# Performance work log

Hardware: AMD Instinct MI355X
Metric: run time of the kernel (lower is better)

## Reference

```python
import jax, jax.numpy as jnp
import numpy as np

N = 50000        # nodes
E = 800000       # edges (avg degree 16)
IN = 256         # in_size
H = 4            # heads
C = 32           # out_size per head
NEG_SLOPE = 0.2  # PyG GATConv leaky_relu slope
LN_EPS = 1e-5


def setup_inputs() -> dict:
    key = jax.random.key(0)
    ks = jax.random.split(key, 6)
    x = jax.random.normal(ks[0], (N, IN), dtype=jnp.float32)
    edge_index = jax.random.randint(ks[1], (2, E), 0, N, dtype=jnp.int32)
    W = jax.random.normal(ks[2], (IN, H * C), dtype=jnp.float32) * 0.05
    att_src = jax.random.normal(ks[3], (H, C), dtype=jnp.float32) * 0.05
    att_dst = jax.random.normal(ks[4], (H, C), dtype=jnp.float32) * 0.05
    bias = jnp.zeros((H * C,), dtype=jnp.float32)
    ln_gamma = jnp.ones((H * C,), dtype=jnp.float32)
    ln_beta = jnp.zeros((H * C,), dtype=jnp.float32)
    return {"x": x, "edge_index": edge_index, "W": W, "att_src": att_src,
            "att_dst": att_dst, "bias": bias, "ln_gamma": ln_gamma,
            "ln_beta": ln_beta}


def _segment_softmax(alpha, seg, num_segments):
    # alpha: [E, H], softmax over edges sharing the same destination node.
    amax = jax.ops.segment_max(alpha, seg, num_segments=num_segments)  # [N, H]
    amax = jnp.where(jnp.isfinite(amax), amax, 0.0)  # nodes with no in-edges
    ex = jnp.exp(alpha - amax[seg])
    denom = jax.ops.segment_sum(ex, seg, num_segments=num_segments)    # [N, H]
    return ex / (denom[seg] + 1e-16)


def reference(x, edge_index, W, att_src, att_dst, bias, ln_gamma, ln_beta):
    # --- GATConv (concat=True) ---
    x_lin = (x @ W).reshape(N, H, C)                    # [N, H, C]
    a_src = jnp.sum(x_lin * att_src, axis=-1)           # [N, H]
    a_dst = jnp.sum(x_lin * att_dst, axis=-1)           # [N, H]
    src, dst = edge_index[0], edge_index[1]             # messages src -> dst
    alpha = a_src[src] + a_dst[dst]                     # [E, H]
    alpha = jnp.where(alpha >= 0, alpha, NEG_SLOPE * alpha)
    alpha = _segment_softmax(alpha, dst, N)             # [E, H]
    msg = x_lin[src] * alpha[..., None]                 # [E, H, C]
    out = jax.ops.segment_sum(msg, dst, num_segments=N) # [N, H, C]
    out = out.reshape(N, H * C) + bias                  # [N, H*C]
    # --- LayerNorm over feature dim ---
    mu = jnp.mean(out, axis=-1, keepdims=True)
    var = jnp.mean(jnp.square(out - mu), axis=-1, keepdims=True)
    out = (out - mu) * jax.lax.rsqrt(var + LN_EPS) * ln_gamma + ln_beta
    # --- activation ---
    return jax.nn.relu(out)
```

## Files before the change

kernel.cpp:

```cpp
#include <hip/hip_runtime.h>

#define NNODES 50000
#define NEDGES 800000
#define INFEAT 256
#define HC 128
#define NH 4
#define CPH 32
#define LSTRIDE 264

typedef unsigned int uint32;
typedef unsigned short u16;
typedef short short8 __attribute__((ext_vector_type(8)));
typedef float f32x4 __attribute__((ext_vector_type(4)));

__device__ __forceinline__ float b2f(u16 s) {
    uint32 u = ((uint32)s) << 16;
    return __builtin_bit_cast(float, u);
}
__device__ __forceinline__ u16 f2bf(float x) {
    uint32 u = __builtin_bit_cast(uint32, x);
    uint32 r = (u + 0x7FFFu + ((u >> 16) & 1u)) >> 16;
    return (u16)r;
}
__device__ __forceinline__ bool probe_bf16(const void* gamma) {
    return ((const uint32*)gamma)[0] == 0x3F803F80u;
}

__global__ __launch_bounds__(256) void wtp_kernel(const void* __restrict__ W,
                                                  const void* __restrict__ gm,
                                                  u16* __restrict__ wtp,
                                                  int* __restrict__ count) {
    const bool isbf = probe_bf16(gm);
    int c = blockIdx.x * 256 + threadIdx.x;
    int kt = c >> 9, nt = (c >> 6) & 7, l = c & 63;
    int r = l & 15, quad = l >> 4;
    int n = nt * 16 + r;
    int kbase = kt * 32 + quad * 8;
    u16 vals[8];
#pragma unroll
    for (int j = 0; j < 8; ++j) {
        int k = kbase + j;
        vals[j] = isbf ? ((const u16*)W)[k * HC + n] : f2bf(((const float*)W)[k * HC + n]);
    }
    *(uint4*)(wtp + (size_t)c * 8) = *(const uint4*)vals;
    for (int i = c; i < NNODES; i += 4096) count[i] = 0;
}

__global__ __launch_bounds__(256) void gemm_mfma(const void* __restrict__ x,
                                                 const uint4* __restrict__ wtp,
                                                 const void* __restrict__ att_src,
                                                 const void* __restrict__ att_dst,
                                                 const void* __restrict__ gm,
                                                 u16* __restrict__ xlin,
                                                 float* __restrict__ asrc,
                                                 float* __restrict__ adst) {
    __shared__ u16 atile[4 * 16 * LSTRIDE];
    const bool isbf = probe_bf16(gm);
    const int tid = threadIdx.x;
    const int wv = tid >> 6;
    const int lane = tid & 63;
    int wave = blockIdx.x * 4 + wv;
    int r = lane & 15;
    int quad = lane >> 4;
    int m0 = wave * 16;
    u16* my = atile + wv * (16 * LSTRIDE);

    if (isbf) {
#pragma unroll
        for (int rep = 0; rep < 8; ++rep) {
            int idx = rep * 64 + lane;
            int row = idx >> 5;
            int ch  = idx & 31;
            int gr = m0 + row;
            if (gr > NNODES - 1) gr = NNODES - 1;
            uint4 q = *(const uint4*)((const u16*)x + (size_t)gr * INFEAT + ch * 8);
            *(uint4*)(my + row * LSTRIDE + ch * 8) = q;
        }
    } else {
#pragma unroll
        for (int rep = 0; rep < 16; ++rep) {
            int idx = rep * 64 + lane;
            int row = idx >> 6;
            int c4  = idx & 63;
            int gr = m0 + row;
            if (gr > NNODES - 1) gr = NNODES - 1;
            float4 f = *(const float4*)((const float*)x + (size_t)gr * INFEAT + c4 * 4);
            u16 v[4] = {f2bf(f.x), f2bf(f.y), f2bf(f.z), f2bf(f.w)};
            *(uint2*)(my + row * LSTRIDE + c4 * 4) = *(const uint2*)v;
        }
    }
    __syncthreads();

    f32x4 acc[8];
#pragma unroll
    for (int nt = 0; nt < 8; ++nt) acc[nt] = (f32x4){0.f, 0.f, 0.f, 0.f};

#pragma unroll
    for (int kt = 0; kt < 8; ++kt) {
        short8 afrag = __builtin_bit_cast(short8,
            *(const uint4*)(my + r * LSTRIDE + kt * 32 + quad * 8));
#pragma unroll
        for (int nt = 0; nt < 8; ++nt) {
            short8 bfrag = __builtin_bit_cast(short8, wtp[(kt * 8 + nt) * 64 + lane]);
            acc[nt] = __builtin_amdgcn_mfma_f32_16x16x32_bf16(afrag, bfrag, acc[nt], 0, 0, 0);
        }
    }
#pragma unroll
    for (int nt = 0; nt < 8; ++nt) {
#pragma unroll
        for (int reg = 0; reg < 4; ++reg) {
            int grow = m0 + quad * 4 + reg;
            if (grow < NNODES) xlin[(size_t)grow * HC + nt * 16 + r] = f2bf(acc[nt][reg]);
        }
    }

    float asv[8], adv[8];
#pragma unroll
    for (int nt = 0; nt < 8; ++nt) {
        int c = nt * 16 + r;
        if (isbf) {
            asv[nt] = b2f(((const u16*)att_src)[c]);
            adv[nt] = b2f(((const u16*)att_dst)[c]);
        } else {
            asv[nt] = ((const float*)att_src)[c];
            adv[nt] = ((const float*)att_dst)[c];
        }
    }
    float psrc[4][4], pdst[4][4];
#pragma unroll
    for (int h = 0; h < 4; ++h)
#pragma unroll
        for (int reg = 0; reg < 4; ++reg) { psrc[h][reg] = 0.f; pdst[h][reg] = 0.f; }
#pragma unroll
    for (int nt = 0; nt < 8; ++nt) {
        const int h = nt >> 1;
#pragma unroll
        for (int reg = 0; reg < 4; ++reg) {
            psrc[h][reg] = fmaf(acc[nt][reg], asv[nt], psrc[h][reg]);
            pdst[h][reg] = fmaf(acc[nt][reg], adv[nt], pdst[h][reg]);
        }
    }
#pragma unroll
    for (int m = 1; m < 16; m <<= 1) {
#pragma unroll
        for (int h = 0; h < 4; ++h)
#pragma unroll
            for (int reg = 0; reg < 4; ++reg) {
                psrc[h][reg] += __shfl_xor(psrc[h][reg], m);
                pdst[h][reg] += __shfl_xor(pdst[h][reg], m);
            }
    }
#pragma unroll
    for (int reg = 0; reg < 4; ++reg)
#pragma unroll
        for (int h = 0; h < 4; ++h)
            if (r == reg * 4 + h) {
                int grow = m0 + quad * 4 + reg;
                if (grow < NNODES) {
                    asrc[grow * 4 + h] = psrc[h][reg];
                    adst[grow * 4 + h] = pdst[h][reg];
                }
            }
}

__global__ __launch_bounds__(256) void hist_kernel(const int* __restrict__ ei,
                                                   int* __restrict__ count,
                                                   int* __restrict__ rank) {
    int e = blockIdx.x * 256 + threadIdx.x;
    if (e < NEDGES) rank[e] = atomicAdd(&count[ei[NEDGES + e]], 1);
}

__global__ __launch_bounds__(256) void blkred_kernel(const int* __restrict__ count,
                                                     int* __restrict__ blksum) {
    int i = blockIdx.x * 256 + threadIdx.x;
    int v = (i < NNODES) ? count[i] : 0;
#pragma unroll
    for (int m = 1; m < 64; m <<= 1) v += __shfl_xor(v, m);
    __shared__ int s[4];
    if ((threadIdx.x & 63) == 0) s[threadIdx.x >> 6] = v;
    __syncthreads();
    if (threadIdx.x == 0) blksum[blockIdx.x] = s[0] + s[1] + s[2] + s[3];
}

__global__ __launch_bounds__(256) void scanout_kernel(const int* __restrict__ count,
                                                      const int* __restrict__ blksum,
                                                      int* __restrict__ offsets) {
    __shared__ int sb[256];
    __shared__ int sd[256];
    const int nblk = (NNODES + 255) / 256;
    int t = threadIdx.x;
    int bv = (t < nblk) ? blksum[t] : 0;
    sb[t] = bv;
    __syncthreads();
    for (int off = 1; off < 256; off <<= 1) {
        int tv = (t >= off) ? sb[t - off] : 0;
        __syncthreads();
        sb[t] += tv;
        __syncthreads();
    }
    int base = sb[blockIdx.x] - blksum[blockIdx.x];

    int i = blockIdx.x * 256 + t;
    int v = (i < NNODES) ? count[i] : 0;
    sd[t] = v;
    __syncthreads();
    for (int off = 1; off < 256; off <<= 1) {
        int tv = (t >= off) ? sd[t - off] : 0;
        __syncthreads();
        sd[t] += tv;
        __syncthreads();
    }
    if (i < NNODES) offsets[i] = base + sd[t] - v;
    if (i == 0) offsets[NNODES] = NEDGES;
}

__global__ __launch_bounds__(256) void scatter_kernel(const int* __restrict__ ei,
                                                      const int* __restrict__ offsets,
                                                      const int* __restrict__ rank,
                                                      int* __restrict__ col) {
    int e = blockIdx.x * 256 + threadIdx.x;
    if (e >= NEDGES) return;
    int d = ei[NEDGES + e];
    col[offsets[d] + rank[e]] = ei[e];
}

__global__ __launch_bounds__(256) void node_kernel(const u16* __restrict__ xlin,
                                                   const float* __restrict__ asrc,
                                                   const float* __restrict__ adst,
                                                   const int* __restrict__ offsets,
                                                   const int* __restrict__ col,
                                                   const void* __restrict__ bias,
                                                   const void* __restrict__ gamma,
                                                   const void* __restrict__ beta,
                                                   void* __restrict__ out) {
    const bool isbf = probe_bf16(gamma);
    int node = blockIdx.x * 4 + (threadIdx.x >> 6);
    int lane = threadIdx.x & 63;
    int h = lane >> 4;
    int f2 = lane * 2;
    float adh = adst[node * 4 + h];
    int start = offsets[node];
    int end = offsets[node + 1];

    float dsum = 0.f, acc0 = 0.f, acc1 = 0.f;
    for (int i = start; i < end; i += 8) {
        int cc[8];
        uint32 pf[8];
        float aw[8];
#pragma unroll
        for (int j = 0; j < 8; ++j) {
            int idx = i + j;
            cc[j] = col[idx < end ? idx : (end - 1)];
        }
#pragma unroll
        for (int j = 0; j < 8; ++j) {
            pf[j] = *(const uint32*)(xlin + (size_t)cc[j] * HC + f2);
            aw[j] = asrc[cc[j] * 4 + h];
        }
#pragma unroll
        for (int j = 0; j < 8; ++j) {
            float a = aw[j] + adh;
            a = (a >= 0.f) ? a : 0.2f * a;
            float w = (i + j < end) ? __expf(a) : 0.f;
            dsum += w;
            float x0 = __builtin_bit_cast(float, pf[j] << 16);
            float x1 = __builtin_bit_cast(float, pf[j] & 0xffff0000u);
            acc0 = fmaf(x0, w, acc0);
            acc1 = fmaf(x1, w, acc1);
        }
    }
    float rden = 1.f / (dsum + 1e-16f);

    float bi0, bi1, g0, g1, be0, be1;
    if (isbf) {
        uint32 bb = ((const uint32*)bias)[lane];
        uint32 gg = ((const uint32*)gamma)[lane];
        uint32 eb = ((const uint32*)beta)[lane];
        bi0 = b2f((u16)(bb & 0xffffu)); bi1 = b2f((u16)(bb >> 16));
        g0  = b2f((u16)(gg & 0xffffu)); g1  = b2f((u16)(gg >> 16));
        be0 = b2f((u16)(eb & 0xffffu)); be1 = b2f((u16)(eb >> 16));
    } else {
        float2 tb = ((const float2*)bias)[lane];
        float2 tg = ((const float2*)gamma)[lane];
        float2 te = ((const float2*)beta)[lane];
        bi0 = tb.x; bi1 = tb.y; g0 = tg.x; g1 = tg.y; be0 = te.x; be1 = te.y;
    }
    float v0 = fmaf(acc0, rden, bi0);
    float v1 = fmaf(acc1, rden, bi1);
    float s2 = v0 + v1;
    float q2 = v0 * v0 + v1 * v1;
#pragma unroll
    for (int m = 1; m < 64; m <<= 1) {
        s2 += __shfl_xor(s2, m);
        q2 += __shfl_xor(q2, m);
    }
    float mean = s2 * (1.f / 128.f);
    float var = q2 * (1.f / 128.f) - mean * mean;
    float inv = rsqrtf(var + 1e-5f);
    float d0 = v0 - mean, d1 = v1 - mean;
    float o0 = fmaxf(fmaf(d0 * inv, g0, be0), 0.f);
    float o1 = fmaxf(fmaf(d1 * inv, g1, be1), 0.f);
    if (isbf) {
        uint32 po = (uint32)f2bf(o0) | ((uint32)f2bf(o1) << 16);
        ((uint32*)out)[(size_t)node * 64 + lane] = po;
    } else {
        float2 po; po.x = o0; po.y = o1;
        ((float2*)out)[(size_t)node * 64 + lane] = po;
    }
}

extern "C" void kernel_launch(void* const* d_in, const int* in_sizes, int n_in,
                              void* d_out, int out_size, void* d_ws, size_t ws_size,
                              hipStream_t stream) {
    const void* x       = d_in[0];
    const int*  ei      = (const int*)d_in[1];
    const void* W       = d_in[2];
    const void* att_src = d_in[3];
    const void* att_dst = d_in[4];
    const void* bias    = d_in[5];
    const void* gamma   = d_in[6];
    const void* beta    = d_in[7];

    char* w = (char*)d_ws;
    size_t off = 0;
    u16* xlin    = (u16*)(w + off);   off += 12800000;
    u16* wtp     = (u16*)(w + off);   off += 65536;
    float* asrc  = (float*)(w + off); off += 800000;
    float* adst  = (float*)(w + off); off += 800000;
    int* count   = (int*)(w + off);   off += 200000;
    int* offsets = (int*)(w + off);   off += 200016;
    int* rank    = (int*)(w + off);   off += 3200000;
    int* blksum  = (int*)(w + off);   off += 1024;
    int* col     = (int*)(w + off);   off += 3200000;

    const int NBLK = (NNODES + 255) / 256;
    wtp_kernel<<<16, 256, 0, stream>>>(W, gamma, wtp, count);
    gemm_mfma<<<(NNODES + 63) / 64, 256, 0, stream>>>(x, (const uint4*)wtp, att_src, att_dst,
                                                      gamma, xlin, asrc, adst);
    hist_kernel<<<(NEDGES + 255) / 256, 256, 0, stream>>>(ei, count, rank);
    blkred_kernel<<<NBLK, 256, 0, stream>>>(count, blksum);
    scanout_kernel<<<NBLK, 256, 0, stream>>>(count, blksum, offsets);
    scatter_kernel<<<(NEDGES + 255) / 256, 256, 0, stream>>>(ei, offsets, rank, col);
    node_kernel<<<NNODES / 4, 256, 0, stream>>>(xlin, asrc, adst, offsets, col,
                                                bias, gamma, beta, d_out);
}
```

Before: 223.5 us.

## Fuse edge histogram into GEMM kernel and add exact-tail loops to aggregation

The separate histogram kernel is removed. Its atomic in-degree counting and rank assignment now run at the end of the GEMM kernel, with each block handling 1024 edges. This saves a launch and lets the atomics overlap with GEMM work, though it lengthens the GEMM kernel's tail. The node aggregation loop no longer pads to multiples of 8 with clamped redundant gathers. It now uses 8-wide, 4-wide and scalar remainder loops, which cuts wasted xlin/asrc loads and removes per-element bounds checks, at the cost of more code.

After: 215.6 us. -3.5%, faster.

```diff
diff --git a/kernel.cpp b/kernel.cpp
--- a/kernel.cpp
+++ b/kernel.cpp
@@ -53,7 +53,10 @@
                                                  const void* __restrict__ gm,
                                                  u16* __restrict__ xlin,
                                                  float* __restrict__ asrc,
-                                                 float* __restrict__ adst) {
+                                                 float* __restrict__ adst,
+                                                 const int* __restrict__ ei,
+                                                 int* __restrict__ count,
+                                                 int* __restrict__ rank) {
     __shared__ u16 atile[4 * 16 * LSTRIDE];
     const bool isbf = probe_bf16(gm);
     const int tid = threadIdx.x;
@@ -161,13 +164,13 @@
                     adst[grow * 4 + h] = pdst[h][reg];
                 }
             }
-}
-
-__global__ __launch_bounds__(256) void hist_kernel(const int* __restrict__ ei,
-                                                   int* __restrict__ count,
-                                                   int* __restrict__ rank) {
-    int e = blockIdx.x * 256 + threadIdx.x;
-    if (e < NEDGES) rank[e] = atomicAdd(&count[ei[NEDGES + e]], 1);
+
+    int eb = blockIdx.x * 1024 + tid;
+#pragma unroll
+    for (int rep = 0; rep < 4; ++rep) {
+        int e = eb + rep * 256;
+        if (e < NEDGES) rank[e] = atomicAdd(&count[ei[NEDGES + e]], 1);
+    }
 }
 
 __global__ __launch_bounds__(256) void blkred_kernel(const int* __restrict__ count,
@@ -243,15 +246,13 @@
     int end = offsets[node + 1];
 
     float dsum = 0.f, acc0 = 0.f, acc1 = 0.f;
-    for (int i = start; i < end; i += 8) {
+    int i = start;
+    for (; i + 7 < end; i += 8) {
         int cc[8];
         uint32 pf[8];
         float aw[8];
 #pragma unroll
-        for (int j = 0; j < 8; ++j) {
-            int idx = i + j;
-            cc[j] = col[idx < end ? idx : (end - 1)];
-        }
+        for (int j = 0; j < 8; ++j) cc[j] = col[i + j];
 #pragma unroll
         for (int j = 0; j < 8; ++j) {
             pf[j] = *(const uint32*)(xlin + (size_t)cc[j] * HC + f2);
@@ -261,13 +262,48 @@
         for (int j = 0; j < 8; ++j) {
             float a = aw[j] + adh;
             a = (a >= 0.f) ? a : 0.2f * a;
-            float w = (i + j < end) ? __expf(a) : 0.f;
+            float w = __expf(a);
             dsum += w;
             float x0 = __builtin_bit_cast(float, pf[j] << 16);
             float x1 = __builtin_bit_cast(float, pf[j] & 0xffff0000u);
             acc0 = fmaf(x0, w, acc0);
             acc1 = fmaf(x1, w, acc1);
         }
+    }
+    for (; i + 3 < end; i += 4) {
+        int cc[4];
+        uint32 pf[4];
+        float aw[4];
+#pragma unroll
+        for (int j = 0; j < 4; ++j) cc[j] = col[i + j];
+#pragma unroll
+        for (int j = 0; j < 4; ++j) {
+            pf[j] = *(const uint32*)(xlin + (size_t)cc[j] * HC + f2);
+            aw[j] = asrc[cc[j] * 4 + h];
+        }
+#pragma unroll
+        for (int j = 0; j < 4; ++j) {
+            float a = aw[j] + adh;
+            a = (a >= 0.f) ? a : 0.2f * a;
+            float w = __expf(a);
+            dsum += w;
+            float x0 = __builtin_bit_cast(float, pf[j] << 16);
+            float x1 = __builtin_bit_cast(float, pf[j] & 0xffff0000u);
+            acc0 = fmaf(x0, w, acc0);
+            acc1 = fmaf(x1, w, acc1);
+        }
+    }
+    for (; i < end; ++i) {
+        int c = col[i];
+        uint32 p = *(const uint32*)(xlin + (size_t)c * HC + f2);
+        float a = asrc[c * 4 + h] + adh;
+        a = (a >= 0.f) ? a : 0.2f * a;
+        float w = __expf(a);
+        dsum += w;
+        float x0 = __builtin_bit_cast(float, p << 16);
+        float x1 = __builtin_bit_cast(float, p & 0xffff0000u);
+        acc0 = fmaf(x0, w, acc0);
+        acc1 = fmaf(x1, w, acc1);
     }
     float rden = 1.f / (dsum + 1e-16f);
 
@@ -336,8 +372,8 @@
     const int NBLK = (NNODES + 255) / 256;
     wtp_kernel<<<16, 256, 0, stream>>>(W, gamma, wtp, count);
     gemm_mfma<<<(NNODES + 63) / 64, 256, 0, stream>>>(x, (const uint4*)wtp, att_src, att_dst,
-                                                      gamma, xlin, asrc, adst);
-    hist_kernel<<<(NEDGES + 255) / 256, 256, 0, stream>>>(ei, count, rank);
+                                                      gamma, xlin, asrc, adst,
+                                                      ei, count, rank);
     blkred_kernel<<<NBLK, 256, 0, stream>>>(count, blksum);
     scanout_kernel<<<NBLK, 256, 0, stream>>>(count, blksum, offsets);
     scatter_kernel<<<(NEDGES + 255) / 256, 256, 0, stream>>>(ei, offsets, rank, col);
```
